# Optimization experiments

Measured on AMD Instinct MI355X. Metric: run time of the kernel, lower is better.

Reference implementation:

```python
import jax, jax.numpy as jnp
import numpy as np

NUM_EXPERTS = 8
IN_FEATURES = 1024
OUT_FEATURES = 1024
TOP_K = 2


def setup_inputs() -> dict:
    key = jax.random.key(0)
    k_x, k_we, k_be, k_wg, k_bg = jax.random.split(key, 5)
    scale_e = 1.0 / np.sqrt(IN_FEATURES)
    x = jax.random.normal(k_x, (4, 2048, IN_FEATURES), dtype=jnp.float32)
    # expert weights stored torch-style [E, out, in], bias [E, out]
    W_experts = jax.random.uniform(k_we, (NUM_EXPERTS, OUT_FEATURES, IN_FEATURES), minval=-scale_e, maxval=scale_e, dtype=jnp.float32)
    b_experts = jax.random.uniform(k_be, (NUM_EXPERTS, OUT_FEATURES), minval=-scale_e, maxval=scale_e, dtype=jnp.float32)
    W_gate = jax.random.uniform(k_wg, (NUM_EXPERTS, IN_FEATURES), minval=-scale_e, maxval=scale_e, dtype=jnp.float32)
    b_gate = jax.random.uniform(k_bg, (NUM_EXPERTS,), minval=-scale_e, maxval=scale_e, dtype=jnp.float32)
    return {"x": x, "W_experts": W_experts, "b_experts": b_experts, "W_gate": W_gate, "b_gate": b_gate}


def reference(x, W_experts, b_experts, W_gate, b_gate):
    B, S, D = x.shape
    x_flat = x.reshape(-1, D)  # [T, D]
    # gating
    gate_logits = x_flat @ W_gate.T + b_gate  # [T, E]
    topk_vals, topk_idxs = jax.lax.top_k(gate_logits, TOP_K)  # [T, K]
    topk_weights = jax.nn.softmax(topk_vals, axis=-1)  # [T, K]
    # dense per-token per-expert weight via one-hot scatter of top-k weights
    one_hot = jax.nn.one_hot(topk_idxs, NUM_EXPERTS, dtype=x.dtype)  # [T, K, E]
    w = jnp.einsum('tke,tk->te', one_hot, topk_weights)  # [T, E]
    # every expert runs densely over all tokens (faithful to source)
    expert_outs = jnp.einsum('td,efd->tef', x_flat, W_experts) + b_experts  # [T, E, F]
    out_flat = jnp.einsum('te,tef->tf', w, expert_outs)  # [T, F]
    return out_flat.reshape(B, S, -1)
```

## Files before the change

### kernel.cpp

```cpp
#include <hip/hip_runtime.h>
#include <hip/hip_bf16.h>
#include <stdint.h>

#define NE 8
#define DK 1024
#define FN 1024
#define NTOK 8192

#define BM 320
#define BN 256
#define BK 64
#define NIT (DK / BK)
#define MT 52

#define HB 32
#define EPB (NTOK * 2 / HB)

#define BUFS 73728
#define BOFF 40960

typedef __attribute__((ext_vector_type(4))) float f32x4;
typedef __attribute__((ext_vector_type(8))) short short8;
typedef __attribute__((ext_vector_type(4))) short short4v;

__device__ __forceinline__ unsigned short f2bf(float f) {
    union { float f; unsigned u; } v; v.f = f;
    unsigned r = v.u;
    unsigned lsb = (r >> 16) & 1u;
    r += 0x7fffu + lsb;
    return (unsigned short)(r >> 16);
}
__device__ __forceinline__ float bf2f(unsigned short u) {
    union { unsigned u; float f; } v; v.u = ((unsigned)u) << 16;
    return v.f;
}

__global__ __launch_bounds__(256) void k_gate(const float* __restrict__ x,
    const float* __restrict__ Wg, const float* __restrict__ bg,
    unsigned short* __restrict__ xb, int* __restrict__ meta_e,
    float* __restrict__ meta_w)
{
    const int lane = threadIdx.x & 63;
    const int t = blockIdx.x * 4 + (threadIdx.x >> 6);

    const f32x4* xr = (const f32x4*)(x + (size_t)t * DK);
    f32x4 xv[4];
#pragma unroll
    for (int c = 0; c < 4; ++c) xv[c] = xr[lane + 64 * c];

    short4v* xbo = (short4v*)(xb + (size_t)t * DK);
#pragma unroll
    for (int c = 0; c < 4; ++c) {
        short4v b;
        b.x = (short)f2bf(xv[c].x); b.y = (short)f2bf(xv[c].y);
        b.z = (short)f2bf(xv[c].z); b.w = (short)f2bf(xv[c].w);
        xbo[lane + 64 * c] = b;
    }

    float acc[NE];
#pragma unroll
    for (int e = 0; e < NE; ++e) {
        const f32x4* wr = (const f32x4*)(Wg + e * DK);
        float a = 0.f;
#pragma unroll
        for (int c = 0; c < 4; ++c) {
            f32x4 wv = wr[lane + 64 * c];
            a += xv[c].x * wv.x + xv[c].y * wv.y + xv[c].z * wv.z + xv[c].w * wv.w;
        }
        acc[e] = a;
    }
#pragma unroll
    for (int e = 0; e < NE; ++e) {
        float a = acc[e];
#pragma unroll
        for (int off = 32; off > 0; off >>= 1) a += __shfl_xor(a, off, 64);
        acc[e] = a;
    }
    if (lane == 0) {
        float v[NE];
#pragma unroll
        for (int e = 0; e < NE; ++e) v[e] = acc[e] + bg[e];
        int b0 = 0; float m0 = v[0];
#pragma unroll
        for (int e = 1; e < NE; ++e) if (v[e] > m0) { m0 = v[e]; b0 = e; }
        int b1 = -1; float m1 = -3.4e38f;
#pragma unroll
        for (int e = 0; e < NE; ++e) if (e != b0 && v[e] > m1) { m1 = v[e]; b1 = e; }
        float r = expf(m1 - m0);
        float s = 1.f + r;
        meta_e[2 * t] = b0; meta_e[2 * t + 1] = b1;
        meta_w[2 * t] = 1.f / s; meta_w[2 * t + 1] = r / s;
    }
}

__global__ __launch_bounds__(256) void k_convw(const float* __restrict__ W,
                                               unsigned short* __restrict__ Wb)
{
    int i = blockIdx.x * 256 + threadIdx.x;
    f32x4 v = ((const f32x4*)W)[i];
    short4v b;
    b.x = (short)f2bf(v.x); b.y = (short)f2bf(v.y);
    b.z = (short)f2bf(v.z); b.w = (short)f2bf(v.w);
    ((short4v*)Wb)[i] = b;
}

__global__ __launch_bounds__(256) void k_hist(const int* __restrict__ meta_e,
                                              int* __restrict__ blockcnt)
{
    __shared__ int lh[NE];
    if (threadIdx.x < NE) lh[threadIdx.x] = 0;
    __syncthreads();
    int base = blockIdx.x * EPB;
#pragma unroll
    for (int k = 0; k < EPB / 256; ++k)
        atomicAdd(&lh[meta_e[base + k * 256 + threadIdx.x]], 1);
    __syncthreads();
    if (threadIdx.x < NE) blockcnt[blockIdx.x * NE + threadIdx.x] = lh[threadIdx.x];
}

__global__ void k_scan(const int* __restrict__ blockcnt, int* __restrict__ seg,
                       int* __restrict__ base)
{
    __shared__ int pre[HB][NE];
    __shared__ int colsum[NE];
    __shared__ int segstart[NE];
    int tid = threadIdx.x;
    if (tid < NE) {
        int run = 0;
        for (int b = 0; b < HB; ++b) { pre[b][tid] = run; run += blockcnt[b * NE + tid]; }
        colsum[tid] = run;
    }
    __syncthreads();
    if (tid == 0) {
        int s = 0;
        for (int e = 0; e < NE; ++e) { segstart[e] = s; seg[e] = s; s += colsum[e]; }
        seg[NE] = s;
    }
    __syncthreads();
    for (int i = tid; i < HB * NE; i += 64) {
        int b = i / NE, e = i % NE;
        base[i] = segstart[e] + pre[b][e];
    }
}

__global__ __launch_bounds__(256) void k_scatter(const int* __restrict__ meta_e,
    const float* __restrict__ meta_w, const int* __restrict__ base,
    int* __restrict__ ridx, float* __restrict__ rw)
{
    __shared__ int lh[NE];
    __shared__ int bb[NE];
    if (threadIdx.x < NE) {
        lh[threadIdx.x] = 0;
        bb[threadIdx.x] = base[blockIdx.x * NE + threadIdx.x];
    }
    __syncthreads();
    int bs = blockIdx.x * EPB;
#pragma unroll
    for (int k = 0; k < EPB / 256; ++k) {
        int i = bs + k * 256 + threadIdx.x;
        int e = meta_e[i];
        int r = atomicAdd(&lh[e], 1);
        int p = bb[e] + r;
        ridx[p] = i;
        rw[p] = meta_w[i];
    }
}

template <int MODE>
__global__ __launch_bounds__(512, 2) void k_gemm(const unsigned short* __restrict__ xb,
    const unsigned short* __restrict__ Wb, const float* __restrict__ be,
    const int* __restrict__ seg, const int* __restrict__ ridx,
    const float* __restrict__ rw, float* __restrict__ out, void* __restrict__ ywv)
{
    __shared__ char Lds[2 * BUFS];

    const int bid = blockIdx.x;
    const int e = bid & 7;
    const int n0 = ((bid >> 3) & 3) * BN;
    const int mt = bid >> 5;
    const int s0 = seg[e];
    const int L = seg[e + 1] - s0;
    const int m0 = mt * BM;
    if (m0 >= L) return;

    const int tid = threadIdx.x;
    const int lane = tid & 63;
    const int wid = tid >> 6;
    const int wm = wid >> 2, wn = wid & 3;

    const int ag = ((tid & 7) ^ ((tid >> 3) & 7)) * 8;
    const unsigned short* asrc[5];
#pragma unroll
    for (int c = 0; c < 5; ++c) {
        int r = c * 64 + (tid >> 3);
        int idx = m0 + r; if (idx >= L) idx = L - 1;
        asrc[c] = xb + (size_t)(ridx[s0 + idx] >> 1) * DK + ag;
    }
    const int bgr = ((tid & 3) ^ ((tid >> 3) & 3)) * 8;
    const unsigned short* bsrc[2];
#pragma unroll
    for (int c = 0; c < 2; ++c) {
        int r = c * 128 + (tid >> 2);
        bsrc[c] = Wb + ((size_t)e * FN + n0 + r) * DK + bgr;
    }

    char* LB = (char*)Lds;

    f32x4 acc[10][4];
#pragma unroll
    for (int i = 0; i < 10; ++i)
#pragma unroll
        for (int j = 0; j < 4; ++j) acc[i][j] = f32x4{0.f, 0.f, 0.f, 0.f};

    const int frow = lane & 15;
    const int fq = lane >> 4;
    int a_off[10][2], b_off[4][2];
#pragma unroll
    for (int mi = 0; mi < 10; ++mi) {
        int r = wm * 160 + mi * 16 + frow;
#pragma unroll
        for (int kk = 0; kk < 2; ++kk)
            a_off[mi][kk] = r * 128 + (((kk * 4 + fq) ^ (r & 7)) * 16);
    }
#pragma unroll
    for (int ni = 0; ni < 4; ++ni) {
        int r = wn * 64 + ni * 16 + frow;
        int sl = fq ^ ((r >> 1) & 3);
#pragma unroll
        for (int kk = 0; kk < 2; ++kk)
            b_off[ni][kk] = BOFF + kk * 16384 + r * 64 + sl * 16;
    }

    auto STAGE_A = [&](int buf, int kt) {
        const int ko = kt * BK;
        char* dst = LB + buf * BUFS + wid * 1024;
#pragma unroll
        for (int c = 0; c < 5; ++c)
            __builtin_amdgcn_global_load_lds(
                (const __attribute__((address_space(1))) void*)(asrc[c] + ko),
                (__attribute__((address_space(3))) void*)(dst + c * 8192), 16, 0, 0);
    };
    auto STAGE_B = [&](int buf, int kt, int kh) {
        const int ko = kt * BK + kh * 32;
        char* dst = LB + buf * BUFS + BOFF + kh * 16384 + wid * 1024;
#pragma unroll
        for (int c = 0; c < 2; ++c)
            __builtin_amdgcn_global_load_lds(
                (const __attribute__((address_space(1))) void*)(bsrc[c] + ko),
                (__attribute__((address_space(3))) void*)(dst + c * 8192), 16, 0, 0);
    };

#define GATE(N) do { asm volatile("s_waitcnt vmcnt(" #N ")" ::: "memory"); \
                     __builtin_amdgcn_s_barrier(); \
                     __builtin_amdgcn_sched_barrier(0); } while (0)
#define BARP  do { __builtin_amdgcn_s_barrier(); \
                   __builtin_amdgcn_sched_barrier(0); } while (0)
#define LGKM0 do { asm volatile("s_waitcnt lgkmcnt(0)" ::: "memory"); \
                   __builtin_amdgcn_sched_barrier(0); } while (0)
#define MFMA5(AF, BF, MLO) do { \
    __builtin_amdgcn_s_setprio(1); \
    _Pragma("unroll") \
    for (int mi = 0; mi < 5; ++mi) { \
        _Pragma("unroll") \
        for (int ni = 0; ni < 4; ++ni) \
            acc[(MLO) + mi][ni] = __builtin_amdgcn_mfma_f32_16x16x32_bf16( \
                AF[mi], BF[ni], acc[(MLO) + mi][ni], 0, 0, 0); \
    } \
    __builtin_amdgcn_s_setprio(0); } while (0)

    STAGE_A(0, 0); STAGE_B(0, 0, 0); STAGE_B(0, 0, 1);
    __builtin_amdgcn_sched_barrier(0);

    for (int t = 0; t < NIT; ++t) {
        const int b = t & 1;
        const char* Cb = LB + b * BUFS;
        const bool st = (t + 1 < NIT);
        short8 b0f[4], b1f[4], af[5];

        GATE(2);
#pragma unroll
        for (int ni = 0; ni < 4; ++ni) b0f[ni] = *(const short8*)(Cb + b_off[ni][0]);
#pragma unroll
        for (int mi = 0; mi < 5; ++mi) af[mi] = *(const short8*)(Cb + a_off[mi][0]);
        if (st) STAGE_A(b ^ 1, t + 1);
        LGKM0;
        MFMA5(af, b0f, 0);

        BARP;
#pragma unroll
        for (int mi = 0; mi < 5; ++mi) af[mi] = *(const short8*)(Cb + a_off[5 + mi][0]);
        if (st) STAGE_B(b ^ 1, t + 1, 0);
        LGKM0;
        MFMA5(af, b0f, 5);

        if (st) { GATE(7); } else { GATE(0); }
#pragma unroll
        for (int ni = 0; ni < 4; ++ni) b1f[ni] = *(const short8*)(Cb + b_off[ni][1]);
#pragma unroll
        for (int mi = 0; mi < 5; ++mi) af[mi] = *(const short8*)(Cb + a_off[mi][1]);
        if (st) STAGE_B(b ^ 1, t + 1, 1);
        LGKM0;
        MFMA5(af, b1f, 0);

        BARP;
#pragma unroll
        for (int mi = 0; mi < 5; ++mi) af[mi] = *(const short8*)(Cb + a_off[5 + mi][1]);
        LGKM0;
        MFMA5(af, b1f, 5);
    }
#undef GATE
#undef BARP
#undef LGKM0
#undef MFMA5

    float bias_n[4];
#pragma unroll
    for (int ni = 0; ni < 4; ++ni)
        bias_n[ni] = be[e * FN + n0 + wn * 64 + ni * 16 + frow];

    const int fq4 = fq * 4;
#pragma unroll
    for (int mi = 0; mi < 10; ++mi) {
        int rl = m0 + wm * 160 + mi * 16 + fq4;
#pragma unroll
        for (int j = 0; j < 4; ++j) {
            int idx = rl + j;
            if (idx < L) {
                float w = rw[s0 + idx];
                int oi = ridx[s0 + idx];
                if (MODE == 0) {
                    float* orow = out + (size_t)(oi >> 1) * FN + n0 + wn * 64 + frow;
#pragma unroll
                    for (int ni = 0; ni < 4; ++ni)
                        atomicAdd(orow + ni * 16, w * (acc[mi][ni][j] + bias_n[ni]));
                } else if (MODE == 1) {
                    short4v pk;
                    pk.x = (short)f2bf(w * (acc[mi][0][j] + bias_n[0]));
                    pk.y = (short)f2bf(w * (acc[mi][1][j] + bias_n[1]));
                    pk.z = (short)f2bf(w * (acc[mi][2][j] + bias_n[2]));
                    pk.w = (short)f2bf(w * (acc[mi][3][j] + bias_n[3]));
                    *(short4v*)((unsigned short*)ywv + (size_t)oi * FN + n0 + wn * 64 + frow * 4) = pk;
                } else {
                    f32x4 pk;
                    pk.x = w * (acc[mi][0][j] + bias_n[0]);
                    pk.y = w * (acc[mi][1][j] + bias_n[1]);
                    pk.z = w * (acc[mi][2][j] + bias_n[2]);
                    pk.w = w * (acc[mi][3][j] + bias_n[3]);
                    *(f32x4*)((float*)ywv + (size_t)oi * FN + n0 + wn * 64 + frow * 4) = pk;
                }
            }
        }
    }
}

__global__ __launch_bounds__(256) void k_combine_bf(const unsigned short* __restrict__ yw,
                                                    float* __restrict__ out)
{
    __shared__ float ls[FN];
    int t = blockIdx.x, i = threadIdx.x;
    const unsigned* r0 = (const unsigned*)(yw + (size_t)(2 * t) * FN);
    const unsigned* r1 = (const unsigned*)(yw + (size_t)(2 * t + 1) * FN);
    unsigned a0 = r0[2 * i], a1 = r0[2 * i + 1];
    unsigned c0 = r1[2 * i], c1 = r1[2 * i + 1];
    float s0 = bf2f((unsigned short)(a0 & 0xffff)) + bf2f((unsigned short)(c0 & 0xffff));
    float s1 = bf2f((unsigned short)(a0 >> 16))    + bf2f((unsigned short)(c0 >> 16));
    float s2 = bf2f((unsigned short)(a1 & 0xffff)) + bf2f((unsigned short)(c1 & 0xffff));
    float s3 = bf2f((unsigned short)(a1 >> 16))    + bf2f((unsigned short)(c1 >> 16));
    int base = (i >> 4) * 64 + (i & 15);
    ls[base +  0] = s0;
    ls[base + 16] = s1;
    ls[base + 32] = s2;
    ls[base + 48] = s3;
    __syncthreads();
    ((f32x4*)(out + (size_t)t * FN))[i] = ((const f32x4*)ls)[i];
}

__global__ __launch_bounds__(256) void k_combine_f32(const float* __restrict__ yw,
                                                     float* __restrict__ out)
{
    __shared__ float ls[FN];
    int t = blockIdx.x, i = threadIdx.x;
    f32x4 a = ((const f32x4*)(yw + (size_t)(2 * t) * FN))[i];
    f32x4 b = ((const f32x4*)(yw + (size_t)(2 * t + 1) * FN))[i];
    f32x4 s = a + b;
    int base = (i >> 4) * 64 + (i & 15);
    ls[base +  0] = s.x;
    ls[base + 16] = s.y;
    ls[base + 32] = s.z;
    ls[base + 48] = s.w;
    __syncthreads();
    ((f32x4*)(out + (size_t)t * FN))[i] = ((const f32x4*)ls)[i];
}

extern "C" void kernel_launch(void* const* d_in, const int* in_sizes, int n_in,
                              void* d_out, int out_size, void* d_ws, size_t ws_size,
                              hipStream_t stream)
{
    const float* x   = (const float*)d_in[0];
    const float* We  = (const float*)d_in[1];
    const float* beb = (const float*)d_in[2];
    const float* Wg  = (const float*)d_in[3];
    const float* bg  = (const float*)d_in[4];
    float* out = (float*)d_out;

    char* ws = (char*)d_ws;
    unsigned short* xb = (unsigned short*)ws;
    unsigned short* Wb = (unsigned short*)(ws + (size_t)(16 << 20));
    size_t off = (size_t)(32 << 20);
    int*   seg      = (int*)(ws + off);   off += 256;
    int*   blockcnt = (int*)(ws + off);   off += HB * NE * 4;
    int*   basebuf  = (int*)(ws + off);   off += HB * NE * 4;
    int*   meta_e   = (int*)(ws + off);   off += (size_t)NTOK * 2 * 4;
    float* meta_w   = (float*)(ws + off); off += (size_t)NTOK * 2 * 4;
    int*   ridxb    = (int*)(ws + off);   off += (size_t)NTOK * 2 * 4;
    float* rwb      = (float*)(ws + off); off += (size_t)NTOK * 2 * 4;
    void*  yw       = (void*)(ws + ((off + 255) & ~(size_t)255));
    size_t yw_base  = (size_t)((off + 255) & ~(size_t)255);

    int mode;
    if (ws_size >= yw_base + (size_t)NTOK * 2 * FN * 2) mode = 1;
    else if (ws_size >= yw_base + (size_t)NTOK * 2 * FN * 4) mode = 2;
    else mode = 0;

    k_gate<<<NTOK / 4, 256, 0, stream>>>(x, Wg, bg, xb, meta_e, meta_w);
    k_convw<<<(NE * FN * DK / 4) / 256, 256, 0, stream>>>(We, Wb);
    k_hist<<<HB, 256, 0, stream>>>(meta_e, blockcnt);
    k_scan<<<1, 64, 0, stream>>>(blockcnt, seg, basebuf);
    k_scatter<<<HB, 256, 0, stream>>>(meta_e, meta_w, basebuf, ridxb, rwb);

    const int nblk = NE * (FN / BN) * MT;
    if (mode == 1) {
        k_gemm<1><<<nblk, 512, 0, stream>>>(xb, Wb, beb, seg, ridxb, rwb, out, yw);
        k_combine_bf<<<NTOK, 256, 0, stream>>>((const unsigned short*)yw, out);
    } else if (mode == 2) {
        k_gemm<2><<<nblk, 512, 0, stream>>>(xb, Wb, beb, seg, ridxb, rwb, out, yw);
        k_combine_f32<<<NTOK, 256, 0, stream>>>((const float*)yw, out);
    } else {
        hipMemsetAsync(d_out, 0, (size_t)NTOK * FN * 4, stream);
        k_gemm<0><<<nblk, 512, 0, stream>>>(xb, Wb, beb, seg, ridxb, rwb, out, yw);
    }
}
```

Before: 88.24 us.

## Split each expert's rows evenly across a fixed grid of GEMM blocks

Replaces the fixed 320-row M tiles (52 tile slots per expert, most exiting early) with eight blocks per expert and N-tile. Each block takes an equal share of that expert's routed rows and walks it in chunks of up to 288 rows, splitting each chunk evenly between the two wave rows. The grid becomes 256 blocks, about one per CU, and per-block row counts no longer depend on how the tile boundary falls. Accumulators shrink to 9x4 tiles, which frees registers. The cost is that uneven expert sizes can still leave some blocks with a second loop iteration. A stages are still issued for 320 rows even when fewer are used.

New measurement: 87.42 us. Within noise of the previous version (-0.9%).

```diff
diff --git a/kernel.cpp b/kernel.cpp
--- a/kernel.cpp
+++ b/kernel.cpp
@@ -7,11 +7,9 @@
 #define FN 1024
 #define NTOK 8192
 
-#define BM 320
 #define BN 256
 #define BK 64
 #define NIT (DK / BK)
-#define MT 52
 
 #define HB 32
 #define EPB (NTOK * 2 / HB)
@@ -180,22 +178,18 @@
     const int mt = bid >> 5;
     const int s0 = seg[e];
     const int L = seg[e + 1] - s0;
-    const int m0 = mt * BM;
-    if (m0 >= L) return;
+    const int lpt = (L + 7) >> 3;
+    int m0 = mt * lpt;
+    const int m_end = (m0 + lpt < L) ? (m0 + lpt) : L;
+    if (m0 >= m_end) return;
 
     const int tid = threadIdx.x;
     const int lane = tid & 63;
     const int wid = tid >> 6;
     const int wm = wid >> 2, wn = wid & 3;
-
-    const int ag = ((tid & 7) ^ ((tid >> 3) & 7)) * 8;
-    const unsigned short* asrc[5];
-#pragma unroll
-    for (int c = 0; c < 5; ++c) {
-        int r = c * 64 + (tid >> 3);
-        int idx = m0 + r; if (idx >= L) idx = L - 1;
-        asrc[c] = xb + (size_t)(ridx[s0 + idx] >> 1) * DK + ag;
-    }
+    const int frow = lane & 15;
+    const int fq = lane >> 4;
+
     const int bgr = ((tid & 3) ^ ((tid >> 3) & 3)) * 8;
     const unsigned short* bsrc[2];
 #pragma unroll
@@ -203,52 +197,63 @@
         int r = c * 128 + (tid >> 2);
         bsrc[c] = Wb + ((size_t)e * FN + n0 + r) * DK + bgr;
     }
+    int b_base[2];
+    {
+        int r = wn * 64 + frow;
+        int sl = fq ^ ((frow >> 1) & 3);
+#pragma unroll
+        for (int kk = 0; kk < 2; ++kk)
+            b_base[kk] = BOFF + kk * 16384 + r * 64 + sl * 16;
+    }
 
     char* LB = (char*)Lds;
-
-    f32x4 acc[10][4];
-#pragma unroll
-    for (int i = 0; i < 10; ++i)
-#pragma unroll
-        for (int j = 0; j < 4; ++j) acc[i][j] = f32x4{0.f, 0.f, 0.f, 0.f};
-
-    const int frow = lane & 15;
-    const int fq = lane >> 4;
-    int a_off[10][2], b_off[4][2];
-#pragma unroll
-    for (int mi = 0; mi < 10; ++mi) {
-        int r = wm * 160 + mi * 16 + frow;
+    const int ag = ((tid & 7) ^ ((tid >> 3) & 7)) * 8;
+
+    float bias_n[4];
+#pragma unroll
+    for (int ni = 0; ni < 4; ++ni)
+        bias_n[ni] = be[e * FN + n0 + wn * 64 + ni * 16 + frow];
+
+    for (; m0 < m_end; m0 += 288) {
+        const int rows = (m_end - m0 < 288) ? (m_end - m0) : 288;
+        const int h = ((rows + 15) >> 4) << 3;
+
+        const unsigned short* asrc[5];
+#pragma unroll
+        for (int c = 0; c < 5; ++c) {
+            int r = c * 64 + (tid >> 3);
+            int idx = m0 + r; if (idx >= m_end) idx = m_end - 1;
+            asrc[c] = xb + (size_t)(ridx[s0 + idx] >> 1) * DK + ag;
+        }
+        int a_base[2];
 #pragma unroll
         for (int kk = 0; kk < 2; ++kk)
-            a_off[mi][kk] = r * 128 + (((kk * 4 + fq) ^ (r & 7)) * 16);
-    }
-#pragma unroll
-    for (int ni = 0; ni < 4; ++ni) {
-        int r = wn * 64 + ni * 16 + frow;
-        int sl = fq ^ ((r >> 1) & 3);
-#pragma unroll
-        for (int kk = 0; kk < 2; ++kk)
-            b_off[ni][kk] = BOFF + kk * 16384 + r * 64 + sl * 16;
-    }
-
-    auto STAGE_A = [&](int buf, int kt) {
-        const int ko = kt * BK;
-        char* dst = LB + buf * BUFS + wid * 1024;
-#pragma unroll
-        for (int c = 0; c < 5; ++c)
-            __builtin_amdgcn_global_load_lds(
-                (const __attribute__((address_space(1))) void*)(asrc[c] + ko),
-                (__attribute__((address_space(3))) void*)(dst + c * 8192), 16, 0, 0);
-    };
-    auto STAGE_B = [&](int buf, int kt, int kh) {
-        const int ko = kt * BK + kh * 32;
-        char* dst = LB + buf * BUFS + BOFF + kh * 16384 + wid * 1024;
-#pragma unroll
-        for (int c = 0; c < 2; ++c)
-            __builtin_amdgcn_global_load_lds(
-                (const __attribute__((address_space(1))) void*)(bsrc[c] + ko),
-                (__attribute__((address_space(3))) void*)(dst + c * 8192), 16, 0, 0);
-    };
+            a_base[kk] = (wm * h + frow) * 128 + (((kk * 4 + fq) ^ (frow & 7)) * 16);
+
+        f32x4 acc[9][4];
+#pragma unroll
+        for (int i = 0; i < 9; ++i)
+#pragma unroll
+            for (int j = 0; j < 4; ++j) acc[i][j] = f32x4{0.f, 0.f, 0.f, 0.f};
+
+        auto STAGE_A = [&](int buf, int kt) {
+            const int ko = kt * BK;
+            char* dst = LB + buf * BUFS + wid * 1024;
+#pragma unroll
+            for (int c = 0; c < 5; ++c)
+                __builtin_amdgcn_global_load_lds(
+                    (const __attribute__((address_space(1))) void*)(asrc[c] + ko),
+                    (__attribute__((address_space(3))) void*)(dst + c * 8192), 16, 0, 0);
+        };
+        auto STAGE_B = [&](int buf, int kt, int kh) {
+            const int ko = kt * BK + kh * 32;
+            char* dst = LB + buf * BUFS + BOFF + kh * 16384 + wid * 1024;
+#pragma unroll
+            for (int c = 0; c < 2; ++c)
+                __builtin_amdgcn_global_load_lds(
+                    (const __attribute__((address_space(1))) void*)(bsrc[c] + ko),
+                    (__attribute__((address_space(3))) void*)(dst + c * 8192), 16, 0, 0);
+        };
 
 #define GATE(N) do { asm volatile("s_waitcnt vmcnt(" #N ")" ::: "memory"); \
                      __builtin_amdgcn_s_barrier(); \
@@ -257,10 +262,10 @@
                    __builtin_amdgcn_sched_barrier(0); } while (0)
 #define LGKM0 do { asm volatile("s_waitcnt lgkmcnt(0)" ::: "memory"); \
                    __builtin_amdgcn_sched_barrier(0); } while (0)
-#define MFMA5(AF, BF, MLO) do { \
+#define MFMA45(AF, BF, MLO, CNT) do { \
     __builtin_amdgcn_s_setprio(1); \
     _Pragma("unroll") \
-    for (int mi = 0; mi < 5; ++mi) { \
+    for (int mi = 0; mi < (CNT); ++mi) { \
         _Pragma("unroll") \
         for (int ni = 0; ni < 4; ++ni) \
             acc[(MLO) + mi][ni] = __builtin_amdgcn_mfma_f32_16x16x32_bf16( \
@@ -268,85 +273,87 @@
     } \
     __builtin_amdgcn_s_setprio(0); } while (0)
 
-    STAGE_A(0, 0); STAGE_B(0, 0, 0); STAGE_B(0, 0, 1);
-    __builtin_amdgcn_sched_barrier(0);
-
-    for (int t = 0; t < NIT; ++t) {
-        const int b = t & 1;
-        const char* Cb = LB + b * BUFS;
-        const bool st = (t + 1 < NIT);
-        short8 b0f[4], b1f[4], af[5];
-
-        GATE(2);
-#pragma unroll
-        for (int ni = 0; ni < 4; ++ni) b0f[ni] = *(const short8*)(Cb + b_off[ni][0]);
-#pragma unroll
-        for (int mi = 0; mi < 5; ++mi) af[mi] = *(const short8*)(Cb + a_off[mi][0]);
-        if (st) STAGE_A(b ^ 1, t + 1);
-        LGKM0;
-        MFMA5(af, b0f, 0);
-
-        BARP;
-#pragma unroll
-        for (int mi = 0; mi < 5; ++mi) af[mi] = *(const short8*)(Cb + a_off[5 + mi][0]);
-        if (st) STAGE_B(b ^ 1, t + 1, 0);
-        LGKM0;
-        MFMA5(af, b0f, 5);
-
-        if (st) { GATE(7); } else { GATE(0); }
-#pragma unroll
-        for (int ni = 0; ni < 4; ++ni) b1f[ni] = *(const short8*)(Cb + b_off[ni][1]);
-#pragma unroll
-        for (int mi = 0; mi < 5; ++mi) af[mi] = *(const short8*)(Cb + a_off[mi][1]);
-        if (st) STAGE_B(b ^ 1, t + 1, 1);
-        LGKM0;
-        MFMA5(af, b1f, 0);
-
-        BARP;
-#pragma unroll
-        for (int mi = 0; mi < 5; ++mi) af[mi] = *(const short8*)(Cb + a_off[5 + mi][1]);
-        LGKM0;
-        MFMA5(af, b1f, 5);
-    }
+        STAGE_A(0, 0); STAGE_B(0, 0, 0); STAGE_B(0, 0, 1);
+        __builtin_amdgcn_sched_barrier(0);
+
+        for (int t = 0; t < NIT; ++t) {
+            const int b = t & 1;
+            const char* Cb = LB + b * BUFS;
+            const bool st = (t + 1 < NIT);
+            short8 b0f[4], b1f[4], af[5];
+
+            GATE(2);
+#pragma unroll
+            for (int ni = 0; ni < 4; ++ni)
+                b0f[ni] = *(const short8*)(Cb + b_base[0] + ni * 1024);
+#pragma unroll
+            for (int mi = 0; mi < 5; ++mi)
+                af[mi] = *(const short8*)(Cb + a_base[0] + mi * 2048);
+            if (st) STAGE_A(b ^ 1, t + 1);
+            LGKM0;
+            MFMA45(af, b0f, 0, 5);
+
+            BARP;
+#pragma unroll
+            for (int mi = 0; mi < 4; ++mi)
+                af[mi] = *(const short8*)(Cb + a_base[0] + (5 + mi) * 2048);
+            if (st) STAGE_B(b ^ 1, t + 1, 0);
+            LGKM0;
+            MFMA45(af, b0f, 5, 4);
+
+            if (st) { GATE(7); } else { GATE(0); }
+#pragma unroll
+            for (int ni = 0; ni < 4; ++ni)
+                b1f[ni] = *(const short8*)(Cb + b_base[1] + ni * 1024);
+#pragma unroll
+            for (int mi = 0; mi < 5; ++mi)
+                af[mi] = *(const short8*)(Cb + a_base[1] + mi * 2048);
+            if (st) STAGE_B(b ^ 1, t + 1, 1);
+            LGKM0;
+            MFMA45(af, b1f, 0, 5);
+
+            BARP;
+#pragma unroll
+            for (int mi = 0; mi < 4; ++mi)
+                af[mi] = *(const short8*)(Cb + a_base[1] + (5 + mi) * 2048);
+            LGKM0;
+            MFMA45(af, b1f, 5, 4);
+        }
 #undef GATE
 #undef BARP
 #undef LGKM0
-#undef MFMA5
-
-    float bias_n[4];
-#pragma unroll
-    for (int ni = 0; ni < 4; ++ni)
-        bias_n[ni] = be[e * FN + n0 + wn * 64 + ni * 16 + frow];
-
-    const int fq4 = fq * 4;
-#pragma unroll
-    for (int mi = 0; mi < 10; ++mi) {
-        int rl = m0 + wm * 160 + mi * 16 + fq4;
-#pragma unroll
-        for (int j = 0; j < 4; ++j) {
-            int idx = rl + j;
-            if (idx < L) {
-                float w = rw[s0 + idx];
-                int oi = ridx[s0 + idx];
-                if (MODE == 0) {
-                    float* orow = out + (size_t)(oi >> 1) * FN + n0 + wn * 64 + frow;
-#pragma unroll
-                    for (int ni = 0; ni < 4; ++ni)
-                        atomicAdd(orow + ni * 16, w * (acc[mi][ni][j] + bias_n[ni]));
-                } else if (MODE == 1) {
-                    short4v pk;
-                    pk.x = (short)f2bf(w * (acc[mi][0][j] + bias_n[0]));
-                    pk.y = (short)f2bf(w * (acc[mi][1][j] + bias_n[1]));
-                    pk.z = (short)f2bf(w * (acc[mi][2][j] + bias_n[2]));
-                    pk.w = (short)f2bf(w * (acc[mi][3][j] + bias_n[3]));
-                    *(short4v*)((unsigned short*)ywv + (size_t)oi * FN + n0 + wn * 64 + frow * 4) = pk;
-                } else {
-                    f32x4 pk;
-                    pk.x = w * (acc[mi][0][j] + bias_n[0]);
-                    pk.y = w * (acc[mi][1][j] + bias_n[1]);
-                    pk.z = w * (acc[mi][2][j] + bias_n[2]);
-                    pk.w = w * (acc[mi][3][j] + bias_n[3]);
-                    *(f32x4*)((float*)ywv + (size_t)oi * FN + n0 + wn * 64 + frow * 4) = pk;
+#undef MFMA45
+
+        const int fq4 = fq * 4;
+#pragma unroll
+        for (int mi = 0; mi < 9; ++mi) {
+#pragma unroll
+            for (int j = 0; j < 4; ++j) {
+                int lr = mi * 16 + fq4 + j;
+                int idx = m0 + wm * h + lr;
+                if (lr < h && idx < m_end) {
+                    float w = rw[s0 + idx];
+                    int oi = ridx[s0 + idx];
+                    if (MODE == 0) {
+                        float* orow = out + (size_t)(oi >> 1) * FN + n0 + wn * 64 + frow;
+#pragma unroll
+                        for (int ni = 0; ni < 4; ++ni)
+                            atomicAdd(orow + ni * 16, w * (acc[mi][ni][j] + bias_n[ni]));
+                    } else if (MODE == 1) {
+                        short4v pk;
+                        pk.x = (short)f2bf(w * (acc[mi][0][j] + bias_n[0]));
+                        pk.y = (short)f2bf(w * (acc[mi][1][j] + bias_n[1]));
+                        pk.z = (short)f2bf(w * (acc[mi][2][j] + bias_n[2]));
+                        pk.w = (short)f2bf(w * (acc[mi][3][j] + bias_n[3]));
+                        *(short4v*)((unsigned short*)ywv + (size_t)oi * FN + n0 + wn * 64 + frow * 4) = pk;
+                    } else {
+                        f32x4 pk;
+                        pk.x = w * (acc[mi][0][j] + bias_n[0]);
+                        pk.y = w * (acc[mi][1][j] + bias_n[1]);
+                        pk.z = w * (acc[mi][2][j] + bias_n[2]);
+                        pk.w = w * (acc[mi][3][j] + bias_n[3]);
+                        *(f32x4*)((float*)ywv + (size_t)oi * FN + n0 + wn * 64 + frow * 4) = pk;
+                    }
                 }
             }
         }
@@ -428,7 +435,7 @@
     k_scan<<<1, 64, 0, stream>>>(blockcnt, seg, basebuf);
     k_scatter<<<HB, 256, 0, stream>>>(meta_e, meta_w, basebuf, ridxb, rwb);
 
-    const int nblk = NE * (FN / BN) * MT;
+    const int nblk = NE * (FN / BN) * 8;
     if (mode == 1) {
         k_gemm<1><<<nblk, 512, 0, stream>>>(xb, Wb, beb, seg, ridxb, rwb, out, yw);
         k_combine_bf<<<NTOK, 256, 0, stream>>>((const unsigned short*)yw, out);
```
